# Optimization experiments

Measured on AMD Instinct MI355X. Metric: run time of the kernel, lower is better.

Reference implementation:

```python
import jax, jax.numpy as jnp
import numpy as np

D_EMB = 1024
N_HEADS = 16
D_HEAD = D_EMB // N_HEADS


def setup_inputs() -> dict:
    key = jax.random.key(0)
    ks = jax.random.split(key, 7)
    B, S = 4, 2048
    scale = 1.0 / np.sqrt(D_EMB)
    return {
        "q": jax.random.normal(ks[0], (B, S, D_EMB), dtype=jnp.float32),
        "k": jax.random.normal(ks[1], (B, S, D_EMB), dtype=jnp.float32),
        "v": jax.random.normal(ks[2], (B, S, D_EMB), dtype=jnp.float32),
        "w_q": jax.random.normal(ks[3], (D_EMB, D_EMB), dtype=jnp.float32) * scale,
        "w_k": jax.random.normal(ks[4], (D_EMB, D_EMB), dtype=jnp.float32) * scale,
        "w_v": jax.random.normal(ks[5], (D_EMB, D_EMB), dtype=jnp.float32) * scale,
        "w_o": jax.random.normal(ks[6], (D_EMB, D_EMB), dtype=jnp.float32) * scale,
    }


def reference(q, k, v, w_q, w_k, w_v, w_o):
    B, S, _ = q.shape
    # Linear projections (nn.Linear stores weight as [out, in]; y = x @ W^T)
    qh = (q @ w_q.T).reshape(B, S, N_HEADS, D_HEAD).transpose(0, 2, 1, 3)  # [B,H,S,Dh]
    kh = (k @ w_k.T).reshape(B, S, N_HEADS, D_HEAD).transpose(0, 2, 1, 3)
    vh = (v @ w_v.T).reshape(B, S, N_HEADS, D_HEAD).transpose(0, 2, 1, 3)
    # Scaled dot-product attention with full [B,H,S,S] score matrix
    scores = jnp.einsum('bhqd,bhkd->bhqk', qh, kh) / jnp.sqrt(
        jnp.asarray(D_HEAD, dtype=qh.dtype))
    attn = jax.nn.softmax(scores, axis=-1)
    x = jnp.einsum('bhqk,bhkd->bhqd', attn, vh)  # [B,H,S,Dh]
    x = x.transpose(0, 2, 1, 3).reshape(B, S, N_HEADS * D_HEAD)
    return x @ w_o.T
```

## Files before the change

kernel.cpp:

```cpp
#include <hip/hip_runtime.h>
#include <stdint.h>

#define S_LEN 2048
#define D_EMBD 1024
#define N_HEADS 16
#define D_HEAD 64
#define B_SZ 4
#define M_TOT (B_SZ * S_LEN)

typedef __bf16 bf16x8 __attribute__((ext_vector_type(8)));
typedef float f32x4 __attribute__((ext_vector_type(4)));
typedef float f32x16 __attribute__((ext_vector_type(16)));
typedef unsigned short u16x8 __attribute__((ext_vector_type(8)));
typedef unsigned int u32x4 __attribute__((ext_vector_type(4)));

__device__ __forceinline__ unsigned short f2bf(float f) {
  unsigned u = __builtin_bit_cast(unsigned, f);
  u += 0x7fffu + ((u >> 16) & 1u);
  return (unsigned short)(u >> 16);
}

__device__ __forceinline__ void async16(const void* g, void* l) {
  __builtin_amdgcn_global_load_lds(
      (const __attribute__((address_space(1))) void*)(uintptr_t)g,
      (__attribute__((address_space(3))) void*)(unsigned)(uintptr_t)l,
      16, 0, 0);
}

__device__ __forceinline__ f32x16 mfma32(bf16x8 a, bf16x8 b, f32x16 c) {
  return __builtin_amdgcn_mfma_f32_32x32x16_bf16(a, b, c, 0, 0, 0);
}

__global__ __launch_bounds__(256) void cast_w4_kernel(
    const float* __restrict__ w0, const float* __restrict__ w1,
    const float* __restrict__ w2, const float* __restrict__ w3,
    unsigned short* __restrict__ out) {
  int i = blockIdx.x * 256 + threadIdx.x;
  int seg = i >> 17;
  int off = i & ((1 << 17) - 1);
  const float* src = (seg == 0) ? w0 : (seg == 1) ? w1 : (seg == 2) ? w2 : w3;
  size_t sb = (size_t)off * 8;
  float4 a = *(const float4*)(src + sb);
  float4 b = *(const float4*)(src + sb + 4);
  u16x8 r;
  r[0] = f2bf(a.x); r[1] = f2bf(a.y); r[2] = f2bf(a.z); r[3] = f2bf(a.w);
  r[4] = f2bf(b.x); r[5] = f2bf(b.y); r[6] = f2bf(b.z); r[7] = f2bf(b.w);
  *(u16x8*)(out + (size_t)i * 8) = r;
}

template <int MODE, bool AFP32>
__global__ __launch_bounds__(256) void gemm_bt(
    const void* __restrict__ Ain, const unsigned short* __restrict__ W,
    void* __restrict__ out, float oscale, int M, int N, int K) {
  const unsigned short* A16 = (const unsigned short*)Ain;
  const float* A32 = (const float*)Ain;
  __shared__ __align__(16) unsigned short As[2][128 * 64];
  __shared__ __align__(16) unsigned short Bs[2][128 * 64];
  const int tid = threadIdx.x;
  const int lane = tid & 63;
  const int w = tid >> 6;
  const int wr = w >> 1, wc = w & 1;
  const int l32 = lane & 31, hi = lane >> 5;

  const int nwg = gridDim.x * gridDim.y;
  const int bid = blockIdx.y * gridDim.x + blockIdx.x;
  const int wg = (bid & 7) * (nwg >> 3) + (bid >> 3);
  const int bm = wg >> 3;
  const int bn = wg & 7;

  f32x16 acc[2][2];
  #pragma unroll
  for (int i = 0; i < 2; i++)
    #pragma unroll
    for (int j = 0; j < 2; j++)
      #pragma unroll
      for (int r = 0; r < 16; r++) acc[i][j][r] = 0.f;

  const int srow = w * 32 + (lane >> 3);
  const int scolsw = ((lane & 7) ^ (lane >> 3)) * 8;

  f32x4 ar[4][2];

  #define LOADA(k0)                                                            \
    do {                                                                       \
      _Pragma("unroll")                                                        \
      for (int p = 0; p < 4; ++p) {                                            \
        const float* srcp =                                                    \
            &A32[(size_t)(bm * 128 + srow + p * 8) * K + (k0) + scolsw];       \
        ar[p][0] = *(const f32x4*)srcp;                                        \
        ar[p][1] = *(const f32x4*)(srcp + 4);                                  \
      }                                                                        \
    } while (0)

  #define WRITEA(b)                                                            \
    do {                                                                       \
      _Pragma("unroll")                                                        \
      for (int p = 0; p < 4; ++p) {                                            \
        unsigned c0, c1, c2, c3;                                               \
        asm("v_cvt_pk_bf16_f32 %0, %1, %2" : "=v"(c0)                          \
            : "v"(ar[p][0][0]), "v"(ar[p][0][1]));                             \
        asm("v_cvt_pk_bf16_f32 %0, %1, %2" : "=v"(c1)                          \
            : "v"(ar[p][0][2]), "v"(ar[p][0][3]));                             \
        asm("v_cvt_pk_bf16_f32 %0, %1, %2" : "=v"(c2)                          \
            : "v"(ar[p][1][0]), "v"(ar[p][1][1]));                             \
        asm("v_cvt_pk_bf16_f32 %0, %1, %2" : "=v"(c3)                          \
            : "v"(ar[p][1][2]), "v"(ar[p][1][3]));                             \
        u32x4 pk = {c0, c1, c2, c3};                                           \
        *(u32x4*)((char*)As[b] + (w * 32 + p * 8) * 128 + lane * 16) = pk;     \
      }                                                                        \
    } while (0)

  #define STAGE_ASYNC(b, k0)                                                   \
    do {                                                                       \
      if constexpr (!AFP32) {                                                  \
        _Pragma("unroll")                                                      \
        for (int p = 0; p < 4; ++p)                                            \
          async16(&A16[(size_t)(bm * 128 + srow + p * 8) * K + (k0) + scolsw], \
                  &As[b][(w * 32 + p * 8) * 64]);                              \
      }                                                                        \
      _Pragma("unroll")                                                        \
      for (int p = 0; p < 4; ++p)                                              \
        async16(&W[(size_t)(bn * 128 + srow + p * 8) * K + (k0) + scolsw],     \
                &Bs[b][(w * 32 + p * 8) * 64]);                                \
    } while (0)

  if constexpr (AFP32) LOADA(0);
  STAGE_ASYNC(0, 0);
  if constexpr (AFP32) WRITEA(0);
  __syncthreads();

  int buf = 0;
  for (int k0 = 0; k0 < K; k0 += 64) {
    const bool more = (k0 + 64 < K);
    if (more) {
      if constexpr (AFP32) LOADA(k0 + 64);
      STAGE_ASYNC(buf ^ 1, k0 + 64);
    }
    #pragma unroll
    for (int ksub = 0; ksub < 4; ++ksub) {
      const int koff = ksub * 32 + hi * 16;
      bf16x8 aA[2], bB[2];
      #pragma unroll
      for (int rb = 0; rb < 2; rb++) {
        int row = wr * 64 + rb * 32 + l32;
        aA[rb] = *(const bf16x8*)((const char*)As[buf] + row * 128 +
                                  (koff ^ ((l32 & 7) << 4)));
      }
      #pragma unroll
      for (int cb = 0; cb < 2; cb++) {
        int row = wc * 64 + cb * 32 + l32;
        bB[cb] = *(const bf16x8*)((const char*)Bs[buf] + row * 128 +
                                  (koff ^ ((l32 & 7) << 4)));
      }
      #pragma unroll
      for (int rb = 0; rb < 2; rb++)
        #pragma unroll
        for (int cb = 0; cb < 2; cb++)
          acc[rb][cb] = mfma32(aA[rb], bB[cb], acc[rb][cb]);
    }
    if (more) { if constexpr (AFP32) WRITEA(buf ^ 1); }
    __syncthreads();
    buf ^= 1;
  }
  #undef LOADA
  #undef WRITEA
  #undef STAGE_ASYNC

  #pragma unroll
  for (int rb = 0; rb < 2; rb++)
    #pragma unroll
    for (int cb = 0; cb < 2; cb++)
      #pragma unroll
      for (int r = 0; r < 16; r++) {
        int row = bm * 128 + wr * 64 + rb * 32 + (r & 3) + 8 * (r >> 2) + 4 * hi;
        int col = bn * 128 + wc * 64 + cb * 32 + l32;
        float v = acc[rb][cb][r] * oscale;
        if constexpr (MODE == 0) {
          size_t idx = ((size_t)((row >> 11) * N_HEADS + (col >> 6)) * S_LEN +
                        (row & (S_LEN - 1))) * D_HEAD + (col & (D_HEAD - 1));
          ((unsigned short*)out)[idx] = f2bf(v);
        } else if constexpr (MODE == 1) {
          ((float*)out)[(size_t)row * N + col] = v;
        } else {
          size_t idx = ((size_t)((row >> 11) * N_HEADS + (col >> 6)) * D_HEAD +
                        (col & (D_HEAD - 1))) * S_LEN + (row & (S_LEN - 1));
          ((unsigned short*)out)[idx] = f2bf(v);
        }
      }
}

__global__ __launch_bounds__(512, 4) void attn_kernel(
    const unsigned short* __restrict__ qh, const unsigned short* __restrict__ kh,
    const unsigned short* __restrict__ vt, unsigned short* __restrict__ xout) {
  __shared__ __align__(16) char smem[66560];
  const int tid = threadIdx.x;
  const int lane = tid & 63;
  const int w = tid >> 6;
  const int l32 = lane & 31;
  const int hi = lane >> 5;

  const int bid = blockIdx.x;
  const int wg = (bid & 7) * 64 + (bid >> 3);
  const int bh = wg >> 3;
  const int qb = (wg & 7) * 256 + w * 32;

  const char* Kb = (const char*)kh + (size_t)bh * S_LEN * D_HEAD * 2;
  const char* Vb = (const char*)vt + (size_t)bh * D_HEAD * S_LEN * 2;
  const unsigned short* Q = qh + (size_t)bh * S_LEN * D_HEAD;

  bf16x8 qf[4];
  #pragma unroll
  for (int ks = 0; ks < 4; ks++)
    qf[ks] = *(const bf16x8*)&Q[(qb + l32) * 64 + ks * 16 + hi * 8];

  f32x16 o0, o1;
  #pragma unroll
  for (int r = 0; r < 16; r++) { o0[r] = 0.f; o1[r] = 0.f; }
  float m2 = -1e30f;
  float lsum = 0.f;

  #define STAGE_K(dstb, t)                                                     \
    do {                                                                       \
      int loff = tid * 16;                                                     \
      int krow = loff >> 7;                                                    \
      async16(Kb + (size_t)(t) * 8192 + (loff ^ ((krow & 7) << 4)),            \
              smem + (dstb) * 8192 + w * 1024);                                \
    } while (0)
  #define STAGE_V(dstb, t)                                                     \
    do {                                                                       \
      int loff = tid * 16;                                                     \
      int d = loff >> 7;                                                       \
      int colb = loff & 127;                                                   \
      async16(Vb + (size_t)d * 4096 + (t) * 128 + (colb ^ ((d & 7) << 4)),     \
              smem + 24576 + (dstb) * 8192 + w * 1024);                        \
    } while (0)

  auto compute = [&](const char* Ks, const char* Vs) __attribute__((always_inline)) {
    f32x16 s0, s1;
    #pragma unroll
    for (int r = 0; r < 16; r++) { s0[r] = 0.f; s1[r] = 0.f; }

    __builtin_amdgcn_s_setprio(1);
    #pragma unroll
    for (int ks = 0; ks < 4; ks++) {
      int row = l32;
      bf16x8 ka = *(const bf16x8*)(Ks + ((row * 128 + ks * 32 + hi * 16) ^
                                         ((row & 7) << 4)));
      s0 = mfma32(ka, qf[ks], s0);
    }
    #pragma unroll
    for (int ks = 0; ks < 4; ks++) {
      int row = 32 + l32;
      bf16x8 ka = *(const bf16x8*)(Ks + ((row * 128 + ks * 32 + hi * 16) ^
                                         ((row & 7) << 4)));
      s1 = mfma32(ka, qf[ks], s1);
    }
    __builtin_amdgcn_s_setprio(0);

    float mx = fmaxf(s0[0], s0[1]);
    #pragma unroll
    for (int r = 2; r < 16; r++) mx = fmaxf(mx, s0[r]);
    #pragma unroll
    for (int r = 0; r < 16; r++) mx = fmaxf(mx, s1[r]);
    mx = fmaxf(mx, __shfl_xor(mx, 32));
    if (__any(mx > m2 + 8.0f)) {
      float mn = fmaxf(m2, mx);
      float sc = __builtin_amdgcn_exp2f(m2 - mn);
      lsum *= sc;
      #pragma unroll
      for (int r = 0; r < 16; r++) { o0[r] *= sc; o1[r] *= sc; }
      m2 = mn;
    }
    float ts = 0.f;
    #pragma unroll
    for (int r = 0; r < 16; r++) {
      s0[r] = __builtin_amdgcn_exp2f(s0[r] - m2);
      s1[r] = __builtin_amdgcn_exp2f(s1[r] - m2);
      ts += s0[r] + s1[r];
    }
    lsum += ts;

    unsigned c[8], e[8];
    #pragma unroll
    for (int t = 0; t < 8; t++) {
      asm("v_cvt_pk_bf16_f32 %0, %1, %2"
          : "=v"(c[t]) : "v"(s0[2 * t]), "v"(s0[2 * t + 1]));
      asm("v_cvt_pk_bf16_f32 %0, %1, %2"
          : "=v"(e[t]) : "v"(s1[2 * t]), "v"(s1[2 * t + 1]));
    }
    asm("v_permlane32_swap_b32 %0, %1" : "+v"(c[0]), "+v"(c[2]));
    asm("v_permlane32_swap_b32 %0, %1" : "+v"(c[1]), "+v"(c[3]));
    asm("v_permlane32_swap_b32 %0, %1" : "+v"(c[4]), "+v"(c[6]));
    asm("v_permlane32_swap_b32 %0, %1" : "+v"(c[5]), "+v"(c[7]));
    asm("v_permlane32_swap_b32 %0, %1" : "+v"(e[0]), "+v"(e[2]));
    asm("v_permlane32_swap_b32 %0, %1" : "+v"(e[1]), "+v"(e[3]));
    asm("v_permlane32_swap_b32 %0, %1" : "+v"(e[4]), "+v"(e[6]));
    asm("v_permlane32_swap_b32 %0, %1" : "+v"(e[5]), "+v"(e[7]));
    u32x4 t0 = {c[0], c[1], c[2], c[3]};
    u32x4 t1 = {c[4], c[5], c[6], c[7]};
    u32x4 t2 = {e[0], e[1], e[2], e[3]};
    u32x4 t3 = {e[4], e[5], e[6], e[7]};
    bf16x8 pa0 = __builtin_bit_cast(bf16x8, t0);
    bf16x8 pa1 = __builtin_bit_cast(bf16x8, t1);
    bf16x8 pa2 = __builtin_bit_cast(bf16x8, t2);
    bf16x8 pa3 = __builtin_bit_cast(bf16x8, t3);

    __builtin_amdgcn_s_setprio(1);
    {
      int row = l32;
      bf16x8 va0 = *(const bf16x8*)(Vs + ((row * 128 + 0 * 32 + hi * 16) ^ ((row & 7) << 4)));
      bf16x8 va1 = *(const bf16x8*)(Vs + ((row * 128 + 1 * 32 + hi * 16) ^ ((row & 7) << 4)));
      bf16x8 va2 = *(const bf16x8*)(Vs + ((row * 128 + 2 * 32 + hi * 16) ^ ((row & 7) << 4)));
      bf16x8 va3 = *(const bf16x8*)(Vs + ((row * 128 + 3 * 32 + hi * 16) ^ ((row & 7) << 4)));
      o0 = mfma32(va0, pa0, o0);
      o0 = mfma32(va1, pa1, o0);
      o0 = mfma32(va2, pa2, o0);
      o0 = mfma32(va3, pa3, o0);
    }
    {
      int row = 32 + l32;
      bf16x8 va0 = *(const bf16x8*)(Vs + ((row * 128 + 0 * 32 + hi * 16) ^ ((row & 7) << 4)));
      bf16x8 va1 = *(const bf16x8*)(Vs + ((row * 128 + 1 * 32 + hi * 16) ^ ((row & 7) << 4)));
      bf16x8 va2 = *(const bf16x8*)(Vs + ((row * 128 + 2 * 32 + hi * 16) ^ ((row & 7) << 4)));
      bf16x8 va3 = *(const bf16x8*)(Vs + ((row * 128 + 3 * 32 + hi * 16) ^ ((row & 7) << 4)));
      o1 = mfma32(va0, pa0, o1);
      o1 = mfma32(va1, pa1, o1);
      o1 = mfma32(va2, pa2, o1);
      o1 = mfma32(va3, pa3, o1);
    }
    __builtin_amdgcn_s_setprio(0);
  };

  STAGE_K(0, 0);
  __builtin_amdgcn_sched_barrier(0);
  STAGE_V(0, 0);
  __builtin_amdgcn_sched_barrier(0);
  STAGE_K(1, 1);
  __builtin_amdgcn_sched_barrier(0);

  int kcur = 0, vcur = 0;
  for (int t = 0; t < S_LEN / 64 - 1; ++t) {
    asm volatile("s_waitcnt vmcnt(1)" ::: "memory");
    __builtin_amdgcn_s_barrier();
    __builtin_amdgcn_sched_barrier(0);
    int vnx = vcur ^ 1;
    STAGE_V(vnx, t + 1);
    __builtin_amdgcn_sched_barrier(0);
    if (t < S_LEN / 64 - 2) {
      int knx = kcur + 2; if (knx >= 3) knx -= 3;
      STAGE_K(knx, t + 2);
    }
    __builtin_amdgcn_sched_barrier(0);
    compute(smem + kcur * 8192, smem + 24576 + vcur * 8192);
    kcur = (kcur == 2) ? 0 : kcur + 1;
    vcur = vnx;
  }
  asm volatile("s_waitcnt vmcnt(0)" ::: "memory");
  __builtin_amdgcn_s_barrier();
  __builtin_amdgcn_sched_barrier(0);
  compute(smem + kcur * 8192, smem + 24576 + vcur * 8192);

  #undef STAGE_K
  #undef STAGE_V

  lsum += __shfl_xor(lsum, 32);
  float inv = 1.0f / lsum;

  __syncthreads();
  float* O = (float*)(smem) + w * (32 * 65);
  #pragma unroll
  for (int r = 0; r < 16; r++) {
    int d = (r & 3) + 8 * (r >> 2) + 4 * hi;
    O[l32 * 65 + d] = o0[r] * inv;
    O[l32 * 65 + 32 + d] = o1[r] * inv;
  }
  __syncthreads();
  const int qr = lane >> 1;
  const int coff = (lane & 1) * 32;
  const int b = bh >> 4, h = bh & 15;
  unsigned short* dst =
      &xout[((size_t)(b * S_LEN) + qb + qr) * D_EMBD + h * 64 + coff];
  #pragma unroll
  for (int t = 0; t < 4; t++) {
    u16x8 rr;
    #pragma unroll
    for (int j = 0; j < 8; j++)
      rr[j] = f2bf(O[qr * 65 + coff + t * 8 + j]);
    *(u16x8*)(dst + t * 8) = rr;
  }
}

extern "C" void kernel_launch(void* const* d_in, const int* in_sizes, int n_in,
                              void* d_out, int out_size, void* d_ws, size_t ws_size,
                              hipStream_t stream) {
  const float* q   = (const float*)d_in[0];
  const float* k   = (const float*)d_in[1];
  const float* v   = (const float*)d_in[2];
  const float* wqf = (const float*)d_in[3];
  const float* wkf = (const float*)d_in[4];
  const float* wvf = (const float*)d_in[5];
  const float* wof = (const float*)d_in[6];

  char* ws = (char*)d_ws;
  unsigned short* qh = (unsigned short*)(ws + (16u << 20));
  unsigned short* kh = (unsigned short*)(ws + (32u << 20));
  unsigned short* vt = (unsigned short*)(ws + (48u << 20));
  unsigned short* ax = (unsigned short*)(ws + (64u << 20));
  unsigned short* wq = (unsigned short*)(ws + (80u << 20));
  unsigned short* wk = wq + (1u << 20);
  unsigned short* wv = wk + (1u << 20);
  unsigned short* wo = wv + (1u << 20);

  const float QSCALE = 0.125f * 1.4426950408889634f;

  cast_w4_kernel<<<2048, 256, 0, stream>>>(wqf, wkf, wvf, wof, wq);

  dim3 gg(D_EMBD / 128, M_TOT / 128);

  gemm_bt<0, true><<<gg, 256, 0, stream>>>(q, wq, qh, QSCALE, M_TOT, D_EMBD, D_EMBD);
  gemm_bt<0, true><<<gg, 256, 0, stream>>>(k, wk, kh, 1.0f, M_TOT, D_EMBD, D_EMBD);
  gemm_bt<2, true><<<gg, 256, 0, stream>>>(v, wv, vt, 1.0f, M_TOT, D_EMBD, D_EMBD);

  attn_kernel<<<512, 512, 0, stream>>>(qh, kh, vt, ax);

  gemm_bt<1, false><<<gg, 256, 0, stream>>>(ax, wo, d_out, 1.0f, M_TOT, D_EMBD, D_EMBD);
}
```

Before: 205.5 us.

## Merge Q/K/V projections into one launch with LDS-staged vectorized stores

The three projection GEMMs become one batched launch, with blockIdx.z selecting the input, weight and output. Outputs are staged through LDS per wave so each lane writes 16-byte vectors instead of scattered 2-byte stores, which matters most for the transposed V layout. The attention softmax max and sum reductions are restructured into trees to shorten dependency chains. A separate out_gemm handles the bf16 output projection. This adds LDS traffic in the epilogue, and the waitcnt-based ordering within each wave must be correct.

Result: faster. 198.9 us (-3.2%).

```diff
diff --git a/kernel.cpp b/kernel.cpp
--- a/kernel.cpp
+++ b/kernel.cpp
@@ -48,19 +48,24 @@
   *(u16x8*)(out + (size_t)i * 8) = r;
 }
 
-template <int MODE, bool AFP32>
-__global__ __launch_bounds__(256) void gemm_bt(
-    const void* __restrict__ Ain, const unsigned short* __restrict__ W,
-    void* __restrict__ out, float oscale, int M, int N, int K) {
-  const unsigned short* A16 = (const unsigned short*)Ain;
-  const float* A32 = (const float*)Ain;
-  __shared__ __align__(16) unsigned short As[2][128 * 64];
-  __shared__ __align__(16) unsigned short Bs[2][128 * 64];
+__global__ __launch_bounds__(256) void proj_gemm(
+    const float* __restrict__ Aq, const float* __restrict__ Ak,
+    const float* __restrict__ Av, const unsigned short* __restrict__ Wbase,
+    unsigned short* __restrict__ Obase, float qscale) {
+  constexpr int K = 1024;
+  __shared__ __align__(16) char smem[65536];
   const int tid = threadIdx.x;
   const int lane = tid & 63;
   const int w = tid >> 6;
   const int wr = w >> 1, wc = w & 1;
   const int l32 = lane & 31, hi = lane >> 5;
+
+  const int z = blockIdx.z;
+  const float* A32 = (z == 0) ? Aq : (z == 1) ? Ak : Av;
+  const unsigned short* W = Wbase + ((size_t)z << 20);
+  unsigned short* out = Obase + ((size_t)z << 23);
+  const float oscale = (z == 0) ? qscale : 1.0f;
+  const bool mode0 = (z < 2);
 
   const int nwg = gridDim.x * gridDim.y;
   const int bid = blockIdx.y * gridDim.x + blockIdx.x;
@@ -106,36 +111,153 @@
         asm("v_cvt_pk_bf16_f32 %0, %1, %2" : "=v"(c3)                          \
             : "v"(ar[p][1][2]), "v"(ar[p][1][3]));                             \
         u32x4 pk = {c0, c1, c2, c3};                                           \
-        *(u32x4*)((char*)As[b] + (w * 32 + p * 8) * 128 + lane * 16) = pk;     \
+        *(u32x4*)(smem + (b) * 16384 + (w * 32 + p * 8) * 128 + lane * 16) = pk; \
       }                                                                        \
     } while (0)
 
-  #define STAGE_ASYNC(b, k0)                                                   \
+  #define STAGE_B(b, k0)                                                       \
     do {                                                                       \
-      if constexpr (!AFP32) {                                                  \
-        _Pragma("unroll")                                                      \
-        for (int p = 0; p < 4; ++p)                                            \
-          async16(&A16[(size_t)(bm * 128 + srow + p * 8) * K + (k0) + scolsw], \
-                  &As[b][(w * 32 + p * 8) * 64]);                              \
-      }                                                                        \
       _Pragma("unroll")                                                        \
       for (int p = 0; p < 4; ++p)                                              \
         async16(&W[(size_t)(bn * 128 + srow + p * 8) * K + (k0) + scolsw],     \
-                &Bs[b][(w * 32 + p * 8) * 64]);                                \
+                smem + 32768 + (b) * 16384 + (w * 32 + p * 8) * 128);          \
     } while (0)
 
-  if constexpr (AFP32) LOADA(0);
-  STAGE_ASYNC(0, 0);
-  if constexpr (AFP32) WRITEA(0);
+  LOADA(0);
+  STAGE_B(0, 0);
+  WRITEA(0);
   __syncthreads();
 
   int buf = 0;
   for (int k0 = 0; k0 < K; k0 += 64) {
     const bool more = (k0 + 64 < K);
     if (more) {
-      if constexpr (AFP32) LOADA(k0 + 64);
-      STAGE_ASYNC(buf ^ 1, k0 + 64);
-    }
+      LOADA(k0 + 64);
+      STAGE_B(buf ^ 1, k0 + 64);
+    }
+    #pragma unroll
+    for (int ksub = 0; ksub < 4; ++ksub) {
+      const int koff = ksub * 32 + hi * 16;
+      bf16x8 aA[2], bB[2];
+      #pragma unroll
+      for (int rb = 0; rb < 2; rb++) {
+        int row = wr * 64 + rb * 32 + l32;
+        aA[rb] = *(const bf16x8*)(smem + buf * 16384 + row * 128 +
+                                  (koff ^ ((l32 & 7) << 4)));
+      }
+      #pragma unroll
+      for (int cb = 0; cb < 2; cb++) {
+        int row = wc * 64 + cb * 32 + l32;
+        bB[cb] = *(const bf16x8*)(smem + 32768 + buf * 16384 + row * 128 +
+                                  (koff ^ ((l32 & 7) << 4)));
+      }
+      #pragma unroll
+      for (int rb = 0; rb < 2; rb++)
+        #pragma unroll
+        for (int cb = 0; cb < 2; cb++)
+          acc[rb][cb] = mfma32(aA[rb], bB[cb], acc[rb][cb]);
+    }
+    if (more) WRITEA(buf ^ 1);
+    __syncthreads();
+    buf ^= 1;
+  }
+  #undef LOADA
+  #undef WRITEA
+  #undef STAGE_B
+
+  unsigned short* Lw = (unsigned short*)(smem + w * 9216);
+  if (mode0) {
+    #pragma unroll
+    for (int rb = 0; rb < 2; rb++)
+      #pragma unroll
+      for (int cb = 0; cb < 2; cb++)
+        #pragma unroll
+        for (int r = 0; r < 16; r++) {
+          int ml = rb * 32 + (r & 3) + 8 * (r >> 2) + 4 * hi;
+          int nl = cb * 32 + l32;
+          Lw[ml * 72 + nl] = f2bf(acc[rb][cb][r] * oscale);
+        }
+  } else {
+    #pragma unroll
+    for (int rb = 0; rb < 2; rb++)
+      #pragma unroll
+      for (int cb = 0; cb < 2; cb++)
+        #pragma unroll
+        for (int r = 0; r < 16; r++) {
+          int ml = rb * 32 + (r & 3) + 8 * (r >> 2) + 4 * hi;
+          int nl = cb * 32 + l32;
+          Lw[nl * 72 + ml] = f2bf(acc[rb][cb][r] * oscale);
+        }
+  }
+  asm volatile("s_waitcnt lgkmcnt(0)" ::: "memory");
+
+  const int rows0 = bm * 128 + wr * 64;
+  const int cols0 = bn * 128 + wc * 64;
+  #pragma unroll
+  for (int c = 0; c < 8; c++) {
+    int task = c * 64 + lane;
+    int i0 = task >> 3;
+    int j0 = (task & 7) * 8;
+    u16x8 vv = *(const u16x8*)&Lw[i0 * 72 + j0];
+    if (mode0) {
+      int row = rows0 + i0, col = cols0 + j0;
+      size_t idx = ((size_t)((row >> 11) * N_HEADS + (col >> 6)) * S_LEN +
+                    (row & (S_LEN - 1))) * D_HEAD + (col & (D_HEAD - 1));
+      *(u16x8*)&out[idx] = vv;
+    } else {
+      int col = cols0 + i0, row = rows0 + j0;
+      size_t idx = ((size_t)((row >> 11) * N_HEADS + (col >> 6)) * D_HEAD +
+                    (col & (D_HEAD - 1))) * S_LEN + (row & (S_LEN - 1));
+      *(u16x8*)&out[idx] = vv;
+    }
+  }
+}
+
+__global__ __launch_bounds__(256) void out_gemm(
+    const unsigned short* __restrict__ A, const unsigned short* __restrict__ W,
+    float* __restrict__ out, int M, int N, int K) {
+  __shared__ __align__(16) unsigned short As[2][128 * 64];
+  __shared__ __align__(16) unsigned short Bs[2][128 * 64];
+  const int tid = threadIdx.x;
+  const int lane = tid & 63;
+  const int w = tid >> 6;
+  const int wr = w >> 1, wc = w & 1;
+  const int l32 = lane & 31, hi = lane >> 5;
+
+  const int nwg = gridDim.x * gridDim.y;
+  const int bid = blockIdx.y * gridDim.x + blockIdx.x;
+  const int wg = (bid & 7) * (nwg >> 3) + (bid >> 3);
+  const int bm = wg >> 3;
+  const int bn = wg & 7;
+
+  f32x16 acc[2][2];
+  #pragma unroll
+  for (int i = 0; i < 2; i++)
+    #pragma unroll
+    for (int j = 0; j < 2; j++)
+      #pragma unroll
+      for (int r = 0; r < 16; r++) acc[i][j][r] = 0.f;
+
+  const int srow = w * 32 + (lane >> 3);
+  const int scolsw = ((lane & 7) ^ (lane >> 3)) * 8;
+
+  #define STAGE_G(b, k0)                                                       \
+    do {                                                                       \
+      _Pragma("unroll")                                                        \
+      for (int p = 0; p < 4; ++p) {                                            \
+        async16(&A[(size_t)(bm * 128 + srow + p * 8) * K + (k0) + scolsw],     \
+                &As[b][(w * 32 + p * 8) * 64]);                                \
+        async16(&W[(size_t)(bn * 128 + srow + p * 8) * K + (k0) + scolsw],     \
+                &Bs[b][(w * 32 + p * 8) * 64]);                                \
+      }                                                                        \
+    } while (0)
+
+  STAGE_G(0, 0);
+  __syncthreads();
+
+  int buf = 0;
+  for (int k0 = 0; k0 < K; k0 += 64) {
+    if (k0 + 64 < K) STAGE_G(buf ^ 1, k0 + 64);
     #pragma unroll
     for (int ksub = 0; ksub < 4; ++ksub) {
       const int koff = ksub * 32 + hi * 16;
@@ -158,13 +280,10 @@
         for (int cb = 0; cb < 2; cb++)
           acc[rb][cb] = mfma32(aA[rb], bB[cb], acc[rb][cb]);
     }
-    if (more) { if constexpr (AFP32) WRITEA(buf ^ 1); }
     __syncthreads();
     buf ^= 1;
   }
-  #undef LOADA
-  #undef WRITEA
-  #undef STAGE_ASYNC
+  #undef STAGE_G
 
   #pragma unroll
   for (int rb = 0; rb < 2; rb++)
@@ -174,18 +293,7 @@
       for (int r = 0; r < 16; r++) {
         int row = bm * 128 + wr * 64 + rb * 32 + (r & 3) + 8 * (r >> 2) + 4 * hi;
         int col = bn * 128 + wc * 64 + cb * 32 + l32;
-        float v = acc[rb][cb][r] * oscale;
-        if constexpr (MODE == 0) {
-          size_t idx = ((size_t)((row >> 11) * N_HEADS + (col >> 6)) * S_LEN +
-                        (row & (S_LEN - 1))) * D_HEAD + (col & (D_HEAD - 1));
-          ((unsigned short*)out)[idx] = f2bf(v);
-        } else if constexpr (MODE == 1) {
-          ((float*)out)[(size_t)row * N + col] = v;
-        } else {
-          size_t idx = ((size_t)((row >> 11) * N_HEADS + (col >> 6)) * D_HEAD +
-                        (col & (D_HEAD - 1))) * S_LEN + (row & (S_LEN - 1));
-          ((unsigned short*)out)[idx] = f2bf(v);
-        }
+        out[(size_t)row * N + col] = acc[rb][cb][r];
       }
 }
 
@@ -257,11 +365,13 @@
     }
     __builtin_amdgcn_s_setprio(0);
 
-    float mx = fmaxf(s0[0], s0[1]);
-    #pragma unroll
-    for (int r = 2; r < 16; r++) mx = fmaxf(mx, s0[r]);
-    #pragma unroll
-    for (int r = 0; r < 16; r++) mx = fmaxf(mx, s1[r]);
+    float m8[8];
+    #pragma unroll
+    for (int t = 0; t < 8; t++)
+      m8[t] = fmaxf(fmaxf(s0[2 * t], s0[2 * t + 1]),
+                    fmaxf(s1[2 * t], s1[2 * t + 1]));
+    float mx = fmaxf(fmaxf(fmaxf(m8[0], m8[1]), fmaxf(m8[2], m8[3])),
+                     fmaxf(fmaxf(m8[4], m8[5]), fmaxf(m8[6], m8[7])));
     mx = fmaxf(mx, __shfl_xor(mx, 32));
     if (__any(mx > m2 + 8.0f)) {
       float mn = fmaxf(m2, mx);
@@ -271,14 +381,17 @@
       for (int r = 0; r < 16; r++) { o0[r] *= sc; o1[r] *= sc; }
       m2 = mn;
     }
-    float ts = 0.f;
     #pragma unroll
     for (int r = 0; r < 16; r++) {
       s0[r] = __builtin_amdgcn_exp2f(s0[r] - m2);
       s1[r] = __builtin_amdgcn_exp2f(s1[r] - m2);
-      ts += s0[r] + s1[r];
-    }
-    lsum += ts;
+    }
+    float p8[8];
+    #pragma unroll
+    for (int t = 0; t < 8; t++)
+      p8[t] = (s0[2 * t] + s0[2 * t + 1]) + (s1[2 * t] + s1[2 * t + 1]);
+    lsum += ((p8[0] + p8[1]) + (p8[2] + p8[3])) +
+            ((p8[4] + p8[5]) + (p8[6] + p8[7]));
 
     unsigned c[8], e[8];
     #pragma unroll
@@ -407,21 +520,16 @@
   unsigned short* vt = (unsigned short*)(ws + (48u << 20));
   unsigned short* ax = (unsigned short*)(ws + (64u << 20));
   unsigned short* wq = (unsigned short*)(ws + (80u << 20));
-  unsigned short* wk = wq + (1u << 20);
-  unsigned short* wv = wk + (1u << 20);
-  unsigned short* wo = wv + (1u << 20);
+  unsigned short* wo = wq + (3u << 20);
 
   const float QSCALE = 0.125f * 1.4426950408889634f;
 
   cast_w4_kernel<<<2048, 256, 0, stream>>>(wqf, wkf, wvf, wof, wq);
 
-  dim3 gg(D_EMBD / 128, M_TOT / 128);
-
-  gemm_bt<0, true><<<gg, 256, 0, stream>>>(q, wq, qh, QSCALE, M_TOT, D_EMBD, D_EMBD);
-  gemm_bt<0, true><<<gg, 256, 0, stream>>>(k, wk, kh, 1.0f, M_TOT, D_EMBD, D_EMBD);
-  gemm_bt<2, true><<<gg, 256, 0, stream>>>(v, wv, vt, 1.0f, M_TOT, D_EMBD, D_EMBD);
+  proj_gemm<<<dim3(8, 64, 3), 256, 0, stream>>>(q, k, v, wq, qh, QSCALE);
 
   attn_kernel<<<512, 512, 0, stream>>>(qh, kh, vt, ax);
 
-  gemm_bt<1, false><<<gg, 256, 0, stream>>>(ax, wo, d_out, 1.0f, M_TOT, D_EMBD, D_EMBD);
-}
+  out_gemm<<<dim3(8, 64), 256, 0, stream>>>(ax, wo, (float*)d_out,
+                                            M_TOT, D_EMBD, D_EMBD);
+}
```
